# Kernel tuning notes

Hardware: AMD Instinct MI355X
Metric: run time of the kernel (lower is better)

Reference implementation:

```python
import jax, jax.numpy as jnp
import numpy as np

LORA_ALPHA = 2.0

def setup_inputs() -> dict:
    key = jax.random.key(0)
    k1, k2, k3, k4 = jax.random.split(key, 4)
    B, S, D_IN, D_OUT, R = 4, 2048, 4096, 4096, 16
    x = jax.random.normal(k1, (B, S, D_IN), dtype=jnp.float32)
    weight = jax.random.normal(k2, (D_OUT, D_IN), dtype=jnp.float32) * (1.0 / np.sqrt(D_IN))
    lora_A = jax.random.normal(k3, (R, D_IN), dtype=jnp.float32) * (1.0 / np.sqrt(D_IN))
    lora_B = jax.random.normal(k4, (D_OUT, R), dtype=jnp.float32) * 0.02
    return {"x": x, "weight": weight, "lora_A": lora_A, "lora_B": lora_B}

def reference(x, weight, lora_A, lora_B):
    # main_out = F.linear(x, weight) = x @ weight.T
    main_out = jnp.einsum('bsd,od->bso', x, weight)
    # Faithful to source: materialize lora_weight = B @ A (out x in), then full linear
    lora_weight = lora_B @ lora_A  # [out, in]
    lora_out = jnp.einsum('bsd,od->bso', x, lora_weight) * LORA_ALPHA
    return main_out + lora_out
```

## Files before the change

kernel.cpp:

```cpp
#include <hip/hip_runtime.h>
#include <stdint.h>

typedef __attribute__((ext_vector_type(8))) short bf16x8;
typedef __attribute__((ext_vector_type(4))) float f32x4;

#define GM 8192
#define GN 4096
#define GK 4096
#define KTILES (GK / 64)

__device__ __forceinline__ unsigned short f2bf(float f) {
  union { float f; unsigned int u; } c; c.f = f;
  unsigned int u = c.u;
  unsigned int r = u + 0x7FFFu + ((u >> 16) & 1u);
  return (unsigned short)(r >> 16);
}

__global__ __launch_bounds__(256) void cvt_x_kernel(const float* __restrict__ x,
                                                    unsigned short* __restrict__ xb) {
  int i = blockIdx.x * 256 + threadIdx.x;
  const float4* p = (const float4*)x + (size_t)i * 2;
  float4 a = p[0], b = p[1];
  unsigned short t[8] = { f2bf(a.x), f2bf(a.y), f2bf(a.z), f2bf(a.w),
                          f2bf(b.x), f2bf(b.y), f2bf(b.z), f2bf(b.w) };
  int4 pk; __builtin_memcpy(&pk, t, 16);
  ((int4*)xb)[i] = pk;
}

__global__ __launch_bounds__(256) void weff_kernel(const float* __restrict__ w,
                                                   const float* __restrict__ lA,
                                                   const float* __restrict__ lB,
                                                   unsigned short* __restrict__ wb) {
  const int K = GK;
  int idx = blockIdx.x * 256 + threadIdx.x;
  int cg = idx & 511;
  int rg = idx >> 9;
  int i0 = cg << 3;
  int o0 = rg << 3;

  float acc[8][8];
#pragma unroll
  for (int r = 0; r < 8; ++r)
#pragma unroll
    for (int c = 0; c < 8; ++c) acc[r][c] = 0.f;

#pragma unroll
  for (int r = 0; r < 16; ++r) {
    float4 a0 = *(const float4*)(lA + (size_t)r * K + i0);
    float4 a1 = *(const float4*)(lA + (size_t)r * K + i0 + 4);
    float av[8] = { a0.x, a0.y, a0.z, a0.w, a1.x, a1.y, a1.z, a1.w };
#pragma unroll
    for (int row = 0; row < 8; ++row) {
      float b = lB[(size_t)(o0 + row) * 16 + r];
#pragma unroll
      for (int c = 0; c < 8; ++c) acc[row][c] += b * av[c];
    }
  }

#pragma unroll
  for (int row = 0; row < 8; ++row) {
    float4 w0 = *(const float4*)(w + (size_t)(o0 + row) * K + i0);
    float4 w1 = *(const float4*)(w + (size_t)(o0 + row) * K + i0 + 4);
    unsigned short t[8] = {
      f2bf(w0.x + 2.0f * acc[row][0]), f2bf(w0.y + 2.0f * acc[row][1]),
      f2bf(w0.z + 2.0f * acc[row][2]), f2bf(w0.w + 2.0f * acc[row][3]),
      f2bf(w1.x + 2.0f * acc[row][4]), f2bf(w1.y + 2.0f * acc[row][5]),
      f2bf(w1.z + 2.0f * acc[row][6]), f2bf(w1.w + 2.0f * acc[row][7]) };
    int4 pk; __builtin_memcpy(&pk, t, 16);
    *(int4*)(wb + (size_t)(o0 + row) * K + i0) = pk;
  }
}


__device__ __forceinline__ void gload16(const unsigned short* g, char* l) {
  __builtin_amdgcn_global_load_lds((__attribute__((address_space(1))) void*)g,
                                   (__attribute__((address_space(3))) void*)l, 16, 0, 0);
}

__device__ __forceinline__ void bar() {
  asm volatile("" ::: "memory");
  __builtin_amdgcn_s_barrier();
  asm volatile("" ::: "memory");
}

#define MFMA_BF16(a, b, c) __builtin_amdgcn_mfma_f32_16x16x32_bf16((a), (b), (c), 0, 0, 0)

template <int HALF>
__device__ __forceinline__ void stage_half(const unsigned short* A, const unsigned short* B,
                                           char* smem, int bm0, int bn0, int w, int lane,
                                           int kt, int buf) {
  int sr, isB;
  if constexpr (HALF == 0)      { sr = w + (w & 4);                   isB = 0; }
  else if constexpr (HALF == 1) { sr = ((w >> 1) << 2) + (w & 1);     isB = 1; }
  else if constexpr (HALF == 2) { sr = ((w >> 1) << 2) + (w & 1) + 2; isB = 1; }
  else                          { sr = w + (w & 4) + 4;               isB = 0; }
  const unsigned short* mat = isB ? B : A;
  const int grow = (isB ? bn0 : bm0) + sr * 16 + (lane >> 2);
  const int gcol = ((lane & 3) * 8) ^ ((lane & 32) ? 16 : 0);
#pragma unroll
  for (int sc = 0; sc < 2; ++sc) {
    const unsigned short* src = mat + (size_t)grow * GK + kt * 64 + sc * 32 + gcol;
    char* dst = smem + (buf << 16) + (isB ? 32768 : 0) + ((sr * 2 + sc) << 10);
    gload16(src, dst);
  }
}

__device__ __forceinline__ bf16x8 ldsA(const char* smem, int buf, int sr, int sc, int foff) {
  return *(const bf16x8*)(smem + (buf << 16) + ((sr * 2 + sc) << 10) + foff);
}
__device__ __forceinline__ bf16x8 ldsB(const char* smem, int buf, int sr, int sc, int foff) {
  return *(const bf16x8*)(smem + (buf << 16) + 32768 + ((sr * 2 + sc) << 10) + foff);
}

__global__ __launch_bounds__(512, 2) void gemm_bt_kernel(const unsigned short* __restrict__ A,
                                                         const unsigned short* __restrict__ B,
                                                         float* __restrict__ C) {
  __shared__ alignas(16) char smem[131072];

  const int t = threadIdx.x, lane = t & 63, w = t >> 6;
  const int wm = w >> 2, wn = w & 3;

  const int bid = blockIdx.x;
  const int wg  = (bid & 7) * (512 / 8) + (bid >> 3);
  const int bx = wg & 15, by = wg >> 4;
  const int bm0 = by * 256, bn0 = bx * 256;

  int foff = (lane & 15) * 64 + ((lane >> 4) << 4);
  foff ^= ((foff >> 9) & 1) << 5;

  stage_half<0>(A, B, smem, bm0, bn0, w, lane, 0, 0);
  stage_half<1>(A, B, smem, bm0, bn0, w, lane, 0, 0);
  stage_half<2>(A, B, smem, bm0, bn0, w, lane, 0, 0);
  stage_half<3>(A, B, smem, bm0, bn0, w, lane, 0, 0);
  stage_half<0>(A, B, smem, bm0, bn0, w, lane, 1, 1);
  asm volatile("s_waitcnt vmcnt(6)" ::: "memory");
  bar();

  f32x4 acc[8][4] = {};
  bf16x8 av[4][2], bv0[2][2], bv1[2][2];

#pragma unroll
  for (int mi = 0; mi < 4; ++mi) {
    av[mi][0] = ldsA(smem, 0, wm * 8 + mi, 0, foff);
    av[mi][1] = ldsA(smem, 0, wm * 8 + mi, 1, foff);
  }
#pragma unroll
  for (int ni = 0; ni < 2; ++ni) {
    bv0[ni][0] = ldsB(smem, 0, wn * 4 + ni, 0, foff);
    bv0[ni][1] = ldsB(smem, 0, wn * 4 + ni, 1, foff);
  }

  for (int kt = 0; kt < KTILES; ++kt) {
    const int cur = kt & 1, nxt = cur ^ 1;
    const bool n1 = (kt + 1 < KTILES);
    const bool n2 = (kt + 2 < KTILES);

    if (n1) {
      stage_half<1>(A, B, smem, bm0, bn0, w, lane, kt + 1, nxt);
      asm volatile("s_waitcnt vmcnt(6)" ::: "memory");
    } else {
      asm volatile("s_waitcnt vmcnt(2)" ::: "memory");
    }
    bar();
#pragma unroll
    for (int ni = 0; ni < 2; ++ni) {
      bv1[ni][0] = ldsB(smem, cur, wn * 4 + 2 + ni, 0, foff);
      bv1[ni][1] = ldsB(smem, cur, wn * 4 + 2 + ni, 1, foff);
    }
    __builtin_amdgcn_sched_barrier(0);
    __builtin_amdgcn_s_setprio(1);
#pragma unroll
    for (int mi = 0; mi < 4; ++mi) {
      acc[mi][0] = MFMA_BF16(av[mi][0], bv0[0][0], acc[mi][0]);
      acc[mi][0] = MFMA_BF16(av[mi][1], bv0[0][1], acc[mi][0]);
      acc[mi][1] = MFMA_BF16(av[mi][0], bv0[1][0], acc[mi][1]);
      acc[mi][1] = MFMA_BF16(av[mi][1], bv0[1][1], acc[mi][1]);
    }
    __builtin_amdgcn_s_setprio(0);

    if (n1) {
      stage_half<2>(A, B, smem, bm0, bn0, w, lane, kt + 1, nxt);
      asm volatile("s_waitcnt vmcnt(6)" ::: "memory");
    } else {
      asm volatile("s_waitcnt vmcnt(0)" ::: "memory");
    }
    bar();
    __builtin_amdgcn_s_setprio(1);
#pragma unroll
    for (int mi = 0; mi < 4; ++mi) {
      acc[mi][2] = MFMA_BF16(av[mi][0], bv1[0][0], acc[mi][2]);
      acc[mi][2] = MFMA_BF16(av[mi][1], bv1[0][1], acc[mi][2]);
      acc[mi][3] = MFMA_BF16(av[mi][0], bv1[1][0], acc[mi][3]);
      acc[mi][3] = MFMA_BF16(av[mi][1], bv1[1][1], acc[mi][3]);
      av[mi][0] = ldsA(smem, cur, wm * 8 + 4 + mi, 0, foff);
      av[mi][1] = ldsA(smem, cur, wm * 8 + 4 + mi, 1, foff);
    }
    __builtin_amdgcn_s_setprio(0);

    if (n1) stage_half<3>(A, B, smem, bm0, bn0, w, lane, kt + 1, nxt);
    bar();
    __builtin_amdgcn_s_setprio(1);
#pragma unroll
    for (int mi = 0; mi < 4; ++mi) {
      acc[4 + mi][2] = MFMA_BF16(av[mi][0], bv1[0][0], acc[4 + mi][2]);
      acc[4 + mi][2] = MFMA_BF16(av[mi][1], bv1[0][1], acc[4 + mi][2]);
      acc[4 + mi][3] = MFMA_BF16(av[mi][0], bv1[1][0], acc[4 + mi][3]);
      acc[4 + mi][3] = MFMA_BF16(av[mi][1], bv1[1][1], acc[4 + mi][3]);
    }
    __builtin_amdgcn_s_setprio(0);

    if (n2) stage_half<0>(A, B, smem, bm0, bn0, w, lane, kt + 2, cur);
    if (n2)      { asm volatile("s_waitcnt vmcnt(6)" ::: "memory"); }
    else if (n1) { asm volatile("s_waitcnt vmcnt(4)" ::: "memory"); }
    bar();
    __builtin_amdgcn_s_setprio(1);
#pragma unroll
    for (int ni = 0; ni < 2; ++ni) {
#pragma unroll
      for (int mi = 0; mi < 4; ++mi) {
        acc[4 + mi][ni] = MFMA_BF16(av[mi][0], bv0[ni][0], acc[4 + mi][ni]);
        acc[4 + mi][ni] = MFMA_BF16(av[mi][1], bv0[ni][1], acc[4 + mi][ni]);
      }
      if (n1) {
        bv0[ni][0] = ldsB(smem, nxt, wn * 4 + ni, 0, foff);
        bv0[ni][1] = ldsB(smem, nxt, wn * 4 + ni, 1, foff);
      }
    }
    if (n1) {
#pragma unroll
      for (int mi = 0; mi < 4; ++mi) {
        av[mi][0] = ldsA(smem, nxt, wm * 8 + mi, 0, foff);
        av[mi][1] = ldsA(smem, nxt, wm * 8 + mi, 1, foff);
      }
    }
    __builtin_amdgcn_s_setprio(0);
  }

  const int orow = (lane >> 4) << 2;
#pragma unroll
  for (int mi = 0; mi < 8; ++mi) {
#pragma unroll
    for (int ni = 0; ni < 4; ++ni) {
      float* cp = C + (size_t)(bm0 + wm * 128 + mi * 16 + orow) * GN
                    + (bn0 + wn * 64 + ni * 16 + (lane & 15));
#pragma unroll
      for (int r = 0; r < 4; ++r)
        cp[(size_t)r * GN] = acc[mi][ni][r];
    }
  }
}

extern "C" void kernel_launch(void* const* d_in, const int* in_sizes, int n_in,
                              void* d_out, int out_size, void* d_ws, size_t ws_size,
                              hipStream_t stream) {
  const float* x  = (const float*)d_in[0];
  const float* w  = (const float*)d_in[1];
  const float* lA = (const float*)d_in[2];
  const float* lB = (const float*)d_in[3];
  float* out = (float*)d_out;

  const int M = GM, N = GN, K = GK;

  unsigned short* xb = (unsigned short*)d_ws;
  unsigned short* wb = xb + (size_t)M * K;

  cvt_x_kernel<<<dim3((M * K / 8) / 256), dim3(256), 0, stream>>>(x, xb);
  weff_kernel<<<dim3((N / 8) * (K / 8) / 256), dim3(256), 0, stream>>>(w, lA, lB, wb);
  gemm_bt_kernel<<<dim3((M / 256) * (N / 256)), dim3(512), 0, stream>>>(xb, wb, out);
}
```

Baseline: 288.1 us.

## Unroll GEMM K-loop by two with compile-time buffers and peeled tail

Replaces the runtime K loop with a templated tile body, unrolled by two so buffer indices and tail conditions are compile-time constants, and peels the last two tiles. It also changes the schedule: LDS fragment loads are no longer interleaved with MFMAs, and each compute phase is followed by an extra barrier, which doubles the barriers per tile. This removes runtime branches and address arithmetic, but the register prefetch overlap with MFMA is reduced and barrier overhead grows.

Measured after the change: 288.6 us. About the same (+0.2%).

```diff
diff --git a/kernel.cpp b/kernel.cpp
--- a/kernel.cpp
+++ b/kernel.cpp
@@ -81,6 +81,14 @@
   asm volatile("" ::: "memory");
   __builtin_amdgcn_s_barrier();
   asm volatile("" ::: "memory");
+}
+
+template <int N>
+__device__ __forceinline__ void vmwait() {
+  if constexpr (N == 0)      asm volatile("s_waitcnt vmcnt(0)" ::: "memory");
+  else if constexpr (N == 2) asm volatile("s_waitcnt vmcnt(2)" ::: "memory");
+  else if constexpr (N == 4) asm volatile("s_waitcnt vmcnt(4)" ::: "memory");
+  else if constexpr (N == 6) asm volatile("s_waitcnt vmcnt(6)" ::: "memory");
 }
 
 #define MFMA_BF16(a, b, c) __builtin_amdgcn_mfma_f32_16x16x32_bf16((a), (b), (c), 0, 0, 0)
@@ -112,6 +120,95 @@
   return *(const bf16x8*)(smem + (buf << 16) + 32768 + ((sr * 2 + sc) << 10) + foff);
 }
 
+template <int CUR, int TAIL>
+__device__ __forceinline__ void ktile_body(const unsigned short* __restrict__ A,
+                                           const unsigned short* __restrict__ B,
+                                           char* smem, int bm0, int bn0, int w, int lane,
+                                           int wm, int wn, int foff, int kt,
+                                           bf16x8 (&av)[4][2], bf16x8 (&bv0)[2][2],
+                                           bf16x8 (&bv1)[2][2], f32x4 (&acc)[8][4]) {
+  constexpr int NXT = CUR ^ 1;
+
+#pragma unroll
+  for (int mi = 0; mi < 4; ++mi) {
+    av[mi][0] = ldsA(smem, CUR, wm * 8 + mi, 0, foff);
+    av[mi][1] = ldsA(smem, CUR, wm * 8 + mi, 1, foff);
+  }
+#pragma unroll
+  for (int ni = 0; ni < 2; ++ni) {
+    bv0[ni][0] = ldsB(smem, CUR, wn * 4 + ni, 0, foff);
+    bv0[ni][1] = ldsB(smem, CUR, wn * 4 + ni, 1, foff);
+  }
+  if constexpr (TAIL < 2) { stage_half<1>(A, B, smem, bm0, bn0, w, lane, kt + 1, NXT); vmwait<6>(); }
+  else                    { vmwait<2>(); }
+  bar();
+  __builtin_amdgcn_s_setprio(1);
+#pragma unroll
+  for (int mi = 0; mi < 4; ++mi) {
+    acc[mi][0] = MFMA_BF16(av[mi][0], bv0[0][0], acc[mi][0]);
+    acc[mi][0] = MFMA_BF16(av[mi][1], bv0[0][1], acc[mi][0]);
+    acc[mi][1] = MFMA_BF16(av[mi][0], bv0[1][0], acc[mi][1]);
+    acc[mi][1] = MFMA_BF16(av[mi][1], bv0[1][1], acc[mi][1]);
+  }
+  __builtin_amdgcn_s_setprio(0);
+  bar();
+
+#pragma unroll
+  for (int ni = 0; ni < 2; ++ni) {
+    bv1[ni][0] = ldsB(smem, CUR, wn * 4 + 2 + ni, 0, foff);
+    bv1[ni][1] = ldsB(smem, CUR, wn * 4 + 2 + ni, 1, foff);
+  }
+  if constexpr (TAIL < 2) { stage_half<2>(A, B, smem, bm0, bn0, w, lane, kt + 1, NXT); vmwait<6>(); }
+  else                    { vmwait<0>(); }
+  bar();
+  __builtin_amdgcn_s_setprio(1);
+#pragma unroll
+  for (int mi = 0; mi < 4; ++mi) {
+    acc[mi][2] = MFMA_BF16(av[mi][0], bv1[0][0], acc[mi][2]);
+    acc[mi][2] = MFMA_BF16(av[mi][1], bv1[0][1], acc[mi][2]);
+    acc[mi][3] = MFMA_BF16(av[mi][0], bv1[1][0], acc[mi][3]);
+    acc[mi][3] = MFMA_BF16(av[mi][1], bv1[1][1], acc[mi][3]);
+  }
+  __builtin_amdgcn_s_setprio(0);
+  bar();
+
+#pragma unroll
+  for (int mi = 0; mi < 4; ++mi) {
+    av[mi][0] = ldsA(smem, CUR, wm * 8 + 4 + mi, 0, foff);
+    av[mi][1] = ldsA(smem, CUR, wm * 8 + 4 + mi, 1, foff);
+  }
+  if constexpr (TAIL < 2) { stage_half<3>(A, B, smem, bm0, bn0, w, lane, kt + 1, NXT); vmwait<6>(); }
+  bar();
+  __builtin_amdgcn_s_setprio(1);
+#pragma unroll
+  for (int mi = 0; mi < 4; ++mi) {
+    acc[4 + mi][2] = MFMA_BF16(av[mi][0], bv1[0][0], acc[4 + mi][2]);
+    acc[4 + mi][2] = MFMA_BF16(av[mi][1], bv1[0][1], acc[4 + mi][2]);
+    acc[4 + mi][3] = MFMA_BF16(av[mi][0], bv1[1][0], acc[4 + mi][3]);
+    acc[4 + mi][3] = MFMA_BF16(av[mi][1], bv1[1][1], acc[4 + mi][3]);
+  }
+  __builtin_amdgcn_s_setprio(0);
+  bar();
+
+  if constexpr (TAIL == 0) {
+    stage_half<0>(A, B, smem, bm0, bn0, w, lane, kt + 2, CUR);
+    vmwait<6>();
+  } else if constexpr (TAIL == 1) {
+    vmwait<4>();
+  }
+  bar();
+  __builtin_amdgcn_s_setprio(1);
+#pragma unroll
+  for (int mi = 0; mi < 4; ++mi) {
+    acc[4 + mi][0] = MFMA_BF16(av[mi][0], bv0[0][0], acc[4 + mi][0]);
+    acc[4 + mi][0] = MFMA_BF16(av[mi][1], bv0[0][1], acc[4 + mi][0]);
+    acc[4 + mi][1] = MFMA_BF16(av[mi][0], bv0[1][0], acc[4 + mi][1]);
+    acc[4 + mi][1] = MFMA_BF16(av[mi][1], bv0[1][1], acc[4 + mi][1]);
+  }
+  __builtin_amdgcn_s_setprio(0);
+  bar();
+}
+
 __global__ __launch_bounds__(512, 2) void gemm_bt_kernel(const unsigned short* __restrict__ A,
                                                          const unsigned short* __restrict__ B,
                                                          float* __restrict__ C) {
@@ -133,108 +230,18 @@
   stage_half<2>(A, B, smem, bm0, bn0, w, lane, 0, 0);
   stage_half<3>(A, B, smem, bm0, bn0, w, lane, 0, 0);
   stage_half<0>(A, B, smem, bm0, bn0, w, lane, 1, 1);
-  asm volatile("s_waitcnt vmcnt(6)" ::: "memory");
+  vmwait<6>();
   bar();
 
   f32x4 acc[8][4] = {};
   bf16x8 av[4][2], bv0[2][2], bv1[2][2];
 
-#pragma unroll
-  for (int mi = 0; mi < 4; ++mi) {
-    av[mi][0] = ldsA(smem, 0, wm * 8 + mi, 0, foff);
-    av[mi][1] = ldsA(smem, 0, wm * 8 + mi, 1, foff);
-  }
-#pragma unroll
-  for (int ni = 0; ni < 2; ++ni) {
-    bv0[ni][0] = ldsB(smem, 0, wn * 4 + ni, 0, foff);
-    bv0[ni][1] = ldsB(smem, 0, wn * 4 + ni, 1, foff);
-  }
-
-  for (int kt = 0; kt < KTILES; ++kt) {
-    const int cur = kt & 1, nxt = cur ^ 1;
-    const bool n1 = (kt + 1 < KTILES);
-    const bool n2 = (kt + 2 < KTILES);
-
-    if (n1) {
-      stage_half<1>(A, B, smem, bm0, bn0, w, lane, kt + 1, nxt);
-      asm volatile("s_waitcnt vmcnt(6)" ::: "memory");
-    } else {
-      asm volatile("s_waitcnt vmcnt(2)" ::: "memory");
-    }
-    bar();
-#pragma unroll
-    for (int ni = 0; ni < 2; ++ni) {
-      bv1[ni][0] = ldsB(smem, cur, wn * 4 + 2 + ni, 0, foff);
-      bv1[ni][1] = ldsB(smem, cur, wn * 4 + 2 + ni, 1, foff);
-    }
-    __builtin_amdgcn_sched_barrier(0);
-    __builtin_amdgcn_s_setprio(1);
-#pragma unroll
-    for (int mi = 0; mi < 4; ++mi) {
-      acc[mi][0] = MFMA_BF16(av[mi][0], bv0[0][0], acc[mi][0]);
-      acc[mi][0] = MFMA_BF16(av[mi][1], bv0[0][1], acc[mi][0]);
-      acc[mi][1] = MFMA_BF16(av[mi][0], bv0[1][0], acc[mi][1]);
-      acc[mi][1] = MFMA_BF16(av[mi][1], bv0[1][1], acc[mi][1]);
-    }
-    __builtin_amdgcn_s_setprio(0);
-
-    if (n1) {
-      stage_half<2>(A, B, smem, bm0, bn0, w, lane, kt + 1, nxt);
-      asm volatile("s_waitcnt vmcnt(6)" ::: "memory");
-    } else {
-      asm volatile("s_waitcnt vmcnt(0)" ::: "memory");
-    }
-    bar();
-    __builtin_amdgcn_s_setprio(1);
-#pragma unroll
-    for (int mi = 0; mi < 4; ++mi) {
-      acc[mi][2] = MFMA_BF16(av[mi][0], bv1[0][0], acc[mi][2]);
-      acc[mi][2] = MFMA_BF16(av[mi][1], bv1[0][1], acc[mi][2]);
-      acc[mi][3] = MFMA_BF16(av[mi][0], bv1[1][0], acc[mi][3]);
-      acc[mi][3] = MFMA_BF16(av[mi][1], bv1[1][1], acc[mi][3]);
-      av[mi][0] = ldsA(smem, cur, wm * 8 + 4 + mi, 0, foff);
-      av[mi][1] = ldsA(smem, cur, wm * 8 + 4 + mi, 1, foff);
-    }
-    __builtin_amdgcn_s_setprio(0);
-
-    if (n1) stage_half<3>(A, B, smem, bm0, bn0, w, lane, kt + 1, nxt);
-    bar();
-    __builtin_amdgcn_s_setprio(1);
-#pragma unroll
-    for (int mi = 0; mi < 4; ++mi) {
-      acc[4 + mi][2] = MFMA_BF16(av[mi][0], bv1[0][0], acc[4 + mi][2]);
-      acc[4 + mi][2] = MFMA_BF16(av[mi][1], bv1[0][1], acc[4 + mi][2]);
-      acc[4 + mi][3] = MFMA_BF16(av[mi][0], bv1[1][0], acc[4 + mi][3]);
-      acc[4 + mi][3] = MFMA_BF16(av[mi][1], bv1[1][1], acc[4 + mi][3]);
-    }
-    __builtin_amdgcn_s_setprio(0);
-
-    if (n2) stage_half<0>(A, B, smem, bm0, bn0, w, lane, kt + 2, cur);
-    if (n2)      { asm volatile("s_waitcnt vmcnt(6)" ::: "memory"); }
-    else if (n1) { asm volatile("s_waitcnt vmcnt(4)" ::: "memory"); }
-    bar();
-    __builtin_amdgcn_s_setprio(1);
-#pragma unroll
-    for (int ni = 0; ni < 2; ++ni) {
-#pragma unroll
-      for (int mi = 0; mi < 4; ++mi) {
-        acc[4 + mi][ni] = MFMA_BF16(av[mi][0], bv0[ni][0], acc[4 + mi][ni]);
-        acc[4 + mi][ni] = MFMA_BF16(av[mi][1], bv0[ni][1], acc[4 + mi][ni]);
-      }
-      if (n1) {
-        bv0[ni][0] = ldsB(smem, nxt, wn * 4 + ni, 0, foff);
-        bv0[ni][1] = ldsB(smem, nxt, wn * 4 + ni, 1, foff);
-      }
-    }
-    if (n1) {
-#pragma unroll
-      for (int mi = 0; mi < 4; ++mi) {
-        av[mi][0] = ldsA(smem, nxt, wm * 8 + mi, 0, foff);
-        av[mi][1] = ldsA(smem, nxt, wm * 8 + mi, 1, foff);
-      }
-    }
-    __builtin_amdgcn_s_setprio(0);
-  }
+  for (int kt = 0; kt < KTILES - 2; kt += 2) {
+    ktile_body<0, 0>(A, B, smem, bm0, bn0, w, lane, wm, wn, foff, kt,     av, bv0, bv1, acc);
+    ktile_body<1, 0>(A, B, smem, bm0, bn0, w, lane, wm, wn, foff, kt + 1, av, bv0, bv1, acc);
+  }
+  ktile_body<0, 1>(A, B, smem, bm0, bn0, w, lane, wm, wn, foff, KTILES - 2, av, bv0, bv1, acc);
+  ktile_body<1, 2>(A, B, smem, bm0, bn0, w, lane, wm, wn, foff, KTILES - 1, av, bv0, bv1, acc);
 
   const int orow = (lane >> 4) << 2;
 #pragma unroll
```
